# Kernel optimization log

Hardware: AMD Instinct MI355X
Metric: run time of the kernel (lower is better)

Reference implementation:

```python
import jax, jax.numpy as jnp
import numpy as np


def setup_inputs() -> dict:
    key = jax.random.key(0)
    k1, k2 = jax.random.split(key)
    B, C, L, K = 128, 64, 4096, 31
    inputData = jax.random.normal(k1, (B, C, L), dtype=jnp.float32)
    # independentChannels=False: kernel = randn(1, C, K) expanded to (C, C, K)
    kernel = jnp.broadcast_to(jax.random.normal(k2, (1, C, K), dtype=jnp.float32), (C, C, K))
    return {"inputData": inputData, "kernel": kernel}


def reference(inputData, kernel):
    B, C, L = inputData.shape
    K = kernel.shape[-1]
    N = L + K - 1          # paddedSequenceLength
    pad = (K - 1) // 2
    # rfft with n=N zero-pads the last dim automatically (norm='backward' is jnp default)
    fourierData = jnp.fft.rfft(inputData, n=N, axis=-1)          # [B, C, N//2+1] complex
    kernelFFT = jnp.fft.rfft(kernel, n=N, axis=-1)               # [C, C, N//2+1] complex
    convFourier = jnp.einsum('oif,bif->bof', kernelFFT, fourierData)
    convData = jnp.fft.irfft(convFourier, n=N, axis=-1)          # [B, C, N]
    return convData[:, :, pad:N - pad]                           # [B, C, L]
```

## Files before the change

kernel.cpp:

```cpp
#include <hip/hip_runtime.h>

#define BATCH 128
#define C 64
#define L 4096
#define K 31

#define NT 256
#define CG 8
#define CPB (C / CG)
#define RW 8
#define WTILE 512
#define BTILE 2048

typedef float floatx4 __attribute__((ext_vector_type(4)));

__device__ __forceinline__ floatx4 ld4(const float* p) {
    return *reinterpret_cast<const floatx4*>(p);
}

__global__ __launch_bounds__(NT, 4)
void computeS_kernel(const float* __restrict__ x,
                     const float* __restrict__ w,
                     float* __restrict__ Sp) {
    const int tid  = threadIdx.x;
    const int wv   = tid >> 6;
    const int lane = tid & 63;
    const int tile = blockIdx.x;
    const int b    = blockIdx.y;
    const int cg   = blockIdx.z;
    const int W0   = tile * BTILE + wv * WTILE;
    const int l0   = W0 + lane * RW;
    const int i0   = cg * CPB;
    const float* xb = x + (long)b * C * L;

    const bool lo   = (lane < 2);
    const bool ln0  = (lane == 0);
    const bool hi   = (lane >= 62);
    const bool ln63 = (lane == 63);
    const bool leftOK  = (W0 > 0);
    const bool rightOK = (W0 + WTILE < L);

    float acc[RW];
#pragma unroll
    for (int r = 0; r < RW; ++r) acc[r] = 0.f;

    floatx4 oa = ld4(xb + (long)i0 * L + l0);
    floatx4 obv = ld4(xb + (long)i0 * L + l0 + 4);

    for (int c = 0; c < CPB; ++c) {
        const int i = i0 + c;
        const float* xi = xb + (long)i * L;

        floatx4 hA0, hA1, hB0, hB1;
        hA0 = 0.f; hA1 = 0.f; hB0 = 0.f; hB1 = 0.f;
        if (lo && leftOK) {
            const float* hp = xi + l0 - 16;
            hA0 = ld4(hp); hA1 = ld4(hp + 4);
            if (ln0) { hB0 = ld4(hp + 8); hB1 = ld4(hp + 12); }
        }
        if (hi && rightOK) {
            const float* hp = xi + W0 + WTILE;
            if (ln63) { hA0 = ld4(hp + 8); hA1 = ld4(hp + 12); hB0 = ld4(hp); hB1 = ld4(hp + 4); }
            else      { hA0 = ld4(hp);     hA1 = ld4(hp + 4); }
        }

        floatx4 na = oa, nb = obv;
        if (c + 1 < CPB) {
            const float* np = xi + L + l0;
            na = ld4(np); nb = ld4(np + 4);
        }

        float own[RW] = {oa.x, oa.y, oa.z, oa.w, obv.x, obv.y, obv.z, obv.w};
        float win[40];
#pragma unroll
        for (int j = 0; j < RW; ++j) {
            win[j]      = __shfl_up(own[j], 2, 64);
            win[8 + j]  = __shfl_up(own[j], 1, 64);
            win[16 + j] = own[j];
            win[24 + j] = __shfl_down(own[j], 1, 64);
            win[32 + j] = __shfl_down(own[j], 2, 64);
        }
        if (lo) {
            win[0] = hA0.x; win[1] = hA0.y; win[2] = hA0.z; win[3] = hA0.w;
            win[4] = hA1.x; win[5] = hA1.y; win[6] = hA1.z; win[7] = hA1.w;
            if (ln0) {
                win[8]  = hB0.x; win[9]  = hB0.y; win[10] = hB0.z; win[11] = hB0.w;
                win[12] = hB1.x; win[13] = hB1.y; win[14] = hB1.z; win[15] = hB1.w;
            }
        }
        if (hi) {
            win[32] = hA0.x; win[33] = hA0.y; win[34] = hA0.z; win[35] = hA0.w;
            win[36] = hA1.x; win[37] = hA1.y; win[38] = hA1.z; win[39] = hA1.w;
            if (ln63) {
                win[24] = hB0.x; win[25] = hB0.y; win[26] = hB0.z; win[27] = hB0.w;
                win[28] = hB1.x; win[29] = hB1.y; win[30] = hB1.z; win[31] = hB1.w;
            }
        }

        const float* wp = w + i * K;
#pragma unroll
        for (int k = 0; k < K; ++k) {
            const float wk = wp[k];
#pragma unroll
            for (int r = 0; r < RW; ++r)
                acc[r] += wk * win[r + 31 - k];
        }

        oa = na; obv = nb;
    }

    floatx4 v0, v1;
    v0.x = acc[0]; v0.y = acc[1]; v0.z = acc[2]; v0.w = acc[3];
    v1.x = acc[4]; v1.y = acc[5]; v1.z = acc[6]; v1.w = acc[7];
    float* sp = Sp + ((long)cg * BATCH + b) * L + l0;
    *reinterpret_cast<floatx4*>(sp) = v0;
    *reinterpret_cast<floatx4*>(sp + 4) = v1;
}

__global__ __launch_bounds__(NT)
void broadcast_kernel(const float* __restrict__ Sp,
                      float* __restrict__ out) {
    const int lane = threadIdx.x & 63;
    const int og   = threadIdx.x >> 6;
    const int b    = blockIdx.y;
    const int l4   = blockIdx.x * 64 + lane;
    const long sbase = (long)b * L + (long)l4 * 4;

    floatx4 v = *reinterpret_cast<const floatx4*>(Sp + sbase);
#pragma unroll
    for (int cg = 1; cg < CG; ++cg)
        v += *reinterpret_cast<const floatx4*>(Sp + (long)cg * BATCH * L + sbase);

    float* ob = out + ((long)b * C + og * 16) * L + (long)l4 * 4;
#pragma unroll
    for (int o = 0; o < 16; ++o)
        __builtin_nontemporal_store(v, reinterpret_cast<floatx4*>(ob + (long)o * L));
}

#define FB_R 4
#define FB_TILE (NT * FB_R)
#define FB_WIN 36
__global__ __launch_bounds__(NT)
void fused_kernel(const float* __restrict__ x,
                  const float* __restrict__ w,
                  float* __restrict__ out) {
    const int tid = threadIdx.x;
    const int tile = blockIdx.x;
    const int b = blockIdx.y;
    const int l0 = tile * FB_TILE + tid * FB_R;
    float acc[FB_R] = {0.f, 0.f, 0.f, 0.f};
    const float* xb = x + (long)b * C * L;
    const bool interior = (l0 >= 16) && (l0 + 20 <= L);
    if (interior) {
        const float* xw = xb + (l0 - 16);
#pragma unroll 2
        for (int i = 0; i < C; ++i) {
            float win[FB_WIN];
            const floatx4* p = reinterpret_cast<const floatx4*>(xw + (long)i * L);
#pragma unroll
            for (int j = 0; j < FB_WIN / 4; ++j)
                reinterpret_cast<floatx4*>(win)[j] = p[j];
            const float* wp = w + i * K;
#pragma unroll
            for (int k = 0; k < K; ++k) {
                const float wk = wp[k];
#pragma unroll
                for (int r = 0; r < FB_R; ++r)
                    acc[r] += wk * win[r + 31 - k];
            }
        }
    } else {
        for (int i = 0; i < C; ++i) {
            const float* xi = xb + (long)i * L;
            float win[FB_WIN];
#pragma unroll
            for (int j = 0; j < FB_WIN; ++j) {
                const int g = l0 - 16 + j;
                win[j] = (g >= 0 && g < L) ? xi[g] : 0.f;
            }
            const float* wp = w + i * K;
#pragma unroll
            for (int k = 0; k < K; ++k) {
                const float wk = wp[k];
#pragma unroll
                for (int r = 0; r < FB_R; ++r)
                    acc[r] += wk * win[r + 31 - k];
            }
        }
    }
    float* op = out + (long)b * C * L + l0;
    floatx4 v; v.x = acc[0]; v.y = acc[1]; v.z = acc[2]; v.w = acc[3];
#pragma unroll
    for (int o = 0; o < C; ++o)
        __builtin_nontemporal_store(v, reinterpret_cast<floatx4*>(op + (long)o * L));
}

extern "C" void kernel_launch(void* const* d_in, const int* in_sizes, int n_in,
                              void* d_out, int out_size, void* d_ws, size_t ws_size,
                              hipStream_t stream) {
    const float* x = (const float*)d_in[0];
    const float* w = (const float*)d_in[1];
    float* out = (float*)d_out;

    const size_t sp_bytes = (size_t)CG * BATCH * L * sizeof(float);
    if (ws_size >= sp_bytes) {
        float* Sp = (float*)d_ws;
        dim3 grid1(L / BTILE, BATCH, CG);
        computeS_kernel<<<grid1, NT, 0, stream>>>(x, w, Sp);
        dim3 grid2(L / 256, BATCH);
        broadcast_kernel<<<grid2, NT, 0, stream>>>(Sp, out);
    } else {
        dim3 grid(L / FB_TILE, BATCH);
        fused_kernel<<<grid, NT, 0, stream>>>(x, w, out);
    }
}
```

Before: 68.08 us.

## Widen per-thread register tile to 16 outputs and split channels into 16 groups

Each lane now computes 16 consecutive outputs instead of 8, so one shuffle distance of 1 is enough to build the 31-tap window, and the halo loads are reduced to the first and last lane only. Each block covers the full sequence length for one batch and one channel group, and channels are split into 16 groups of 4 with a fully unrolled channel loop. This cuts shuffle and halo overhead per output, but doubles the partial-sum buffer the broadcast kernel must read and reduce, and raises register pressure under launch bounds of 4 blocks per SM.

```diff
diff --git a/kernel.cpp b/kernel.cpp
--- a/kernel.cpp
+++ b/kernel.cpp
@@ -6,11 +6,10 @@
 #define K 31
 
 #define NT 256
-#define CG 8
+#define CG 16
 #define CPB (C / CG)
-#define RW 8
-#define WTILE 512
-#define BTILE 2048
+#define RW 16
+#define WTILE 1024
 
 typedef float floatx4 __attribute__((ext_vector_type(4)));
 
@@ -25,17 +24,14 @@
     const int tid  = threadIdx.x;
     const int wv   = tid >> 6;
     const int lane = tid & 63;
-    const int tile = blockIdx.x;
-    const int b    = blockIdx.y;
-    const int cg   = blockIdx.z;
-    const int W0   = tile * BTILE + wv * WTILE;
+    const int b    = blockIdx.x;
+    const int cg   = blockIdx.y;
+    const int W0   = wv * WTILE;
     const int l0   = W0 + lane * RW;
     const int i0   = cg * CPB;
     const float* xb = x + (long)b * C * L;
 
-    const bool lo   = (lane < 2);
     const bool ln0  = (lane == 0);
-    const bool hi   = (lane >= 62);
     const bool ln63 = (lane == 63);
     const bool leftOK  = (W0 > 0);
     const bool rightOK = (W0 + WTILE < L);
@@ -44,57 +40,54 @@
 #pragma unroll
     for (int r = 0; r < RW; ++r) acc[r] = 0.f;
 
-    floatx4 oa = ld4(xb + (long)i0 * L + l0);
-    floatx4 obv = ld4(xb + (long)i0 * L + l0 + 4);
-
+    floatx4 h0 = 0.f, h1 = 0.f, h2 = 0.f, h3 = 0.f;
+
+    const float* p0 = xb + (long)i0 * L + l0;
+    floatx4 o0 = ld4(p0), o1 = ld4(p0 + 4), o2 = ld4(p0 + 8), o3 = ld4(p0 + 12);
+
+#pragma unroll
     for (int c = 0; c < CPB; ++c) {
         const int i = i0 + c;
         const float* xi = xb + (long)i * L;
 
-        floatx4 hA0, hA1, hB0, hB1;
-        hA0 = 0.f; hA1 = 0.f; hB0 = 0.f; hB1 = 0.f;
-        if (lo && leftOK) {
-            const float* hp = xi + l0 - 16;
-            hA0 = ld4(hp); hA1 = ld4(hp + 4);
-            if (ln0) { hB0 = ld4(hp + 8); hB1 = ld4(hp + 12); }
-        }
-        if (hi && rightOK) {
+        if (ln0 && leftOK) {
+            const float* hp = xi + W0 - 16;
+            h0 = ld4(hp); h1 = ld4(hp + 4); h2 = ld4(hp + 8); h3 = ld4(hp + 12);
+        }
+        if (ln63 && rightOK) {
             const float* hp = xi + W0 + WTILE;
-            if (ln63) { hA0 = ld4(hp + 8); hA1 = ld4(hp + 12); hB0 = ld4(hp); hB1 = ld4(hp + 4); }
-            else      { hA0 = ld4(hp);     hA1 = ld4(hp + 4); }
-        }
-
-        floatx4 na = oa, nb = obv;
+            h0 = ld4(hp); h1 = ld4(hp + 4); h2 = ld4(hp + 8); h3 = ld4(hp + 12);
+        }
+
+        floatx4 n0 = o0, n1 = o1, n2 = o2, n3 = o3;
         if (c + 1 < CPB) {
             const float* np = xi + L + l0;
-            na = ld4(np); nb = ld4(np + 4);
-        }
-
-        float own[RW] = {oa.x, oa.y, oa.z, oa.w, obv.x, obv.y, obv.z, obv.w};
-        float win[40];
+            n0 = ld4(np); n1 = ld4(np + 4); n2 = ld4(np + 8); n3 = ld4(np + 12);
+        }
+
+        float win[48];
+        *reinterpret_cast<floatx4*>(&win[16]) = o0;
+        *reinterpret_cast<floatx4*>(&win[20]) = o1;
+        *reinterpret_cast<floatx4*>(&win[24]) = o2;
+        *reinterpret_cast<floatx4*>(&win[28]) = o3;
 #pragma unroll
         for (int j = 0; j < RW; ++j) {
-            win[j]      = __shfl_up(own[j], 2, 64);
-            win[8 + j]  = __shfl_up(own[j], 1, 64);
-            win[16 + j] = own[j];
-            win[24 + j] = __shfl_down(own[j], 1, 64);
-            win[32 + j] = __shfl_down(own[j], 2, 64);
-        }
-        if (lo) {
-            win[0] = hA0.x; win[1] = hA0.y; win[2] = hA0.z; win[3] = hA0.w;
-            win[4] = hA1.x; win[5] = hA1.y; win[6] = hA1.z; win[7] = hA1.w;
-            if (ln0) {
-                win[8]  = hB0.x; win[9]  = hB0.y; win[10] = hB0.z; win[11] = hB0.w;
-                win[12] = hB1.x; win[13] = hB1.y; win[14] = hB1.z; win[15] = hB1.w;
-            }
-        }
-        if (hi) {
-            win[32] = hA0.x; win[33] = hA0.y; win[34] = hA0.z; win[35] = hA0.w;
-            win[36] = hA1.x; win[37] = hA1.y; win[38] = hA1.z; win[39] = hA1.w;
-            if (ln63) {
-                win[24] = hB0.x; win[25] = hB0.y; win[26] = hB0.z; win[27] = hB0.w;
-                win[28] = hB1.x; win[29] = hB1.y; win[30] = hB1.z; win[31] = hB1.w;
-            }
+            const float oj = win[16 + j];
+            if (j > 0)  win[j]      = __shfl_up(oj, 1, 64);
+            if (j < 15) win[32 + j] = __shfl_down(oj, 1, 64);
+        }
+        win[0] = 0.f; win[47] = 0.f;
+        if (ln0) {
+            *reinterpret_cast<floatx4*>(&win[0])  = h0;
+            *reinterpret_cast<floatx4*>(&win[4])  = h1;
+            *reinterpret_cast<floatx4*>(&win[8])  = h2;
+            *reinterpret_cast<floatx4*>(&win[12]) = h3;
+        }
+        if (ln63) {
+            *reinterpret_cast<floatx4*>(&win[32]) = h0;
+            *reinterpret_cast<floatx4*>(&win[36]) = h1;
+            *reinterpret_cast<floatx4*>(&win[40]) = h2;
+            *reinterpret_cast<floatx4*>(&win[44]) = h3;
         }
 
         const float* wp = w + i * K;
@@ -106,15 +99,16 @@
                 acc[r] += wk * win[r + 31 - k];
         }
 
-        oa = na; obv = nb;
-    }
-
-    floatx4 v0, v1;
-    v0.x = acc[0]; v0.y = acc[1]; v0.z = acc[2]; v0.w = acc[3];
-    v1.x = acc[4]; v1.y = acc[5]; v1.z = acc[6]; v1.w = acc[7];
+        o0 = n0; o1 = n1; o2 = n2; o3 = n3;
+    }
+
     float* sp = Sp + ((long)cg * BATCH + b) * L + l0;
-    *reinterpret_cast<floatx4*>(sp) = v0;
-    *reinterpret_cast<floatx4*>(sp + 4) = v1;
+#pragma unroll
+    for (int r = 0; r < RW; r += 4) {
+        floatx4 v;
+        v.x = acc[r]; v.y = acc[r + 1]; v.z = acc[r + 2]; v.w = acc[r + 3];
+        *reinterpret_cast<floatx4*>(sp + r) = v;
+    }
 }
 
 __global__ __launch_bounds__(NT)
@@ -205,7 +199,7 @@
     const size_t sp_bytes = (size_t)CG * BATCH * L * sizeof(float);
     if (ws_size >= sp_bytes) {
         float* Sp = (float*)d_ws;
-        dim3 grid1(L / BTILE, BATCH, CG);
+        dim3 grid1(BATCH, CG);
         computeS_kernel<<<grid1, NT, 0, stream>>>(x, w, Sp);
         dim3 grid2(L / 256, BATCH);
         broadcast_kernel<<<grid2, NT, 0, stream>>>(Sp, out);
```

Result: slower. 144.5 us (+112.2%).
